# Kernel optimization log

Measured on AMD Instinct MI355X. Metric: run time of the kernel, lower is better.

Reference implementation:

```python
import jax, jax.numpy as jnp
import numpy as np

WINDOW = 8
NUM_HEADS = 12


def setup_inputs() -> dict:
    key = jax.random.key(0)
    k1, k2, k3 = jax.random.split(key, 3)
    B, H, W, C = 32, 64, 64, 384
    x = jax.random.normal(k1, (B, H, W, C), dtype=jnp.float32)
    w_qkv = jax.random.normal(k2, (C, 3 * C), dtype=jnp.float32) * (C ** -0.5)
    w_proj = jax.random.normal(k3, (C, C), dtype=jnp.float32) * (C ** -0.5)
    b_proj = jnp.zeros((C,), dtype=jnp.float32)
    return {"x": x, "w_qkv": w_qkv, "w_proj": w_proj, "b_proj": b_proj}


def window_partition(x, ws):
    B, H, W, C = x.shape
    x = x.reshape(B, H // ws, ws, W // ws, ws, C)
    x = x.transpose(0, 1, 3, 2, 4, 5)  # [B, nH, nW, ws, ws, C]
    return x.reshape(-1, ws * ws, C)


def window_reverse(x, ws, H, W):
    nWin = (H // ws) * (W // ws)
    B = x.shape[0] // nWin
    C = x.shape[2]
    x = x.reshape(B, H // ws, W // ws, ws, ws, C)
    x = x.transpose(0, 1, 3, 2, 4, 5)
    return x.reshape(B, H, W, C)


def reference(x, w_qkv, w_proj, b_proj):
    B, H, W, C = x.shape
    ws = WINDOW
    nh = NUM_HEADS
    hd = C // nh
    scale = hd ** -0.5
    N = ws * ws

    xw = window_partition(x, ws)                      # [nW*B, N, C]
    qkv = xw @ w_qkv                                  # [nW*B, N, 3C]
    qkv = qkv.reshape(-1, N, 3, nh, hd)
    qkv = qkv.transpose(2, 0, 3, 1, 4)                # [3, nW*B, nh, N, hd]
    q, k, v = qkv[0], qkv[1], qkv[2]

    attn = jnp.einsum('whnd,whmd->whnm', q, k) * scale  # [nW*B, nh, N, N]
    attn = jax.nn.softmax(attn, axis=-1)
    out = jnp.einsum('whnm,whmd->whnd', attn, v)         # [nW*B, nh, N, hd]
    out = out.transpose(0, 2, 1, 3).reshape(-1, N, C)    # [nW*B, N, C]
    out = out @ w_proj + b_proj
    return window_reverse(out, ws, H, W)
```

## Files before the change

### kernel.cpp

```cpp
#include <hip/hip_runtime.h>


typedef __attribute__((ext_vector_type(8))) short bf16x8;
typedef __attribute__((ext_vector_type(4))) float f32x4;
typedef __attribute__((ext_vector_type(4))) short short4_t;

__device__ __forceinline__ short f2bf(float f) {
    union { float f; unsigned u; } v; v.f = f;
    unsigned r = v.u + 0x7fffu + ((v.u >> 16) & 1u);
    return (short)(r >> 16);
}

__device__ __forceinline__ unsigned pk2(float a, float b) {
    return ((unsigned)(unsigned short)f2bf(b) << 16) | (unsigned short)f2bf(a);
}

__device__ __forceinline__ f32x4 mfma16(bf16x8 a, bf16x8 b, f32x4 c) {
    return __builtin_amdgcn_mfma_f32_16x16x32_bf16(a, b, c, 0, 0, 0);
}

__device__ __forceinline__ short4_t pack4(f32x4 v) {
    short4_t s;
    s.x = f2bf(v[0]); s.y = f2bf(v[1]); s.z = f2bf(v[2]); s.w = f2bf(v[3]);
    return s;
}

__device__ __forceinline__ void gload_lds16(const void* g, void* l) {
    __builtin_amdgcn_global_load_lds(
        (const __attribute__((address_space(1))) unsigned int*)g,
        (__attribute__((address_space(3))) unsigned int*)l, 16, 0, 0);
}

__global__ void prep_weights(const float* __restrict__ wqkv, const float* __restrict__ wproj,
                             short* __restrict__ wq_sw, short* __restrict__ wp_t) {
    const int QKV_ELEMS = 12 * 96 * 384;
    int i = blockIdx.x * 256 + threadIdx.x;
    if (i < QKV_ELEMS) {
        int h = i / (96 * 384);
        int o = i % (96 * 384);
        int row = o / 384;
        int kb = ((o % 384) * 2) ^ ((row & 7) << 4);
        int k = kb >> 1;
        int col = (row >> 5) * 384 + h * 32 + (row & 31);
        float w = wqkv[k * 1152 + col];
        if (row < 32) w *= 0.17677669529663687f;
        wq_sw[i] = f2bf(w);
    } else if (i < QKV_ELEMS + 384 * 384) {
        int j = i - QKV_ELEMS;
        int n = j / 384, k = j % 384;
        wp_t[j] = f2bf(wproj[k * 384 + n]);
    }
}

__global__ __launch_bounds__(1024, 4)
void qkv_attn(const float* __restrict__ x, const short* __restrict__ wq_sw,
              short* __restrict__ y_sw) {
    __shared__ short Wl[96 * 384];
    __shared__ short k_s[4][64 * 44];
    __shared__ short v_t[4][32 * 76];
    __shared__ short ps[4][64 * 76];

    const int tid   = threadIdx.x;
    const int lane  = tid & 63;
    const int wid   = tid >> 6;
    const int col16 = lane & 15;
    const int kgrp  = lane >> 4;
    const int w     = wid >> 2;
    const int quad  = wid & 3;

    const int win = blockIdx.x * 4 + w;
    const int b = win >> 6, wi = win & 63, whr = wi >> 3, wwc = wi & 7;
    const float* xbase = x + (((b * 64) + whr * 8) * 64 + wwc * 8) * 384;

    for (int i = wid; i < 72; i += 16)
        gload_lds16(wq_sw + i * 512 + lane * 8, &Wl[i * 512]);

    bf16x8 xf[12];
    {
        int t = quad * 16 + col16;
        const float* xr = xbase + ((t >> 3) * 64 + (t & 7)) * 384;
#pragma unroll
        for (int kk = 0; kk < 12; ++kk) {
            const float* p0 = xr + kk * 32 + kgrp * 8;
            float4 a = *reinterpret_cast<const float4*>(p0);
            float4 c = *reinterpret_cast<const float4*>(p0 + 4);
            bf16x8 f;
            f[0] = f2bf(a.x); f[1] = f2bf(a.y); f[2] = f2bf(a.z); f[3] = f2bf(a.w);
            f[4] = f2bf(c.x); f[5] = f2bf(c.y); f[6] = f2bf(c.z); f[7] = f2bf(c.w);
            xf[kk] = f;
        }
    }

    const int g = win * 64 + quad * 16 + col16;
    const int mtile = g >> 7, yrow = g & 127;
    char* ybase = (char*)y_sw + (size_t)mtile * 98304 + (size_t)yrow * 128;

    for (int h = 0; h < 12; ++h) {
        __syncthreads();

        f32x4 acc[6];
#pragma unroll
        for (int i = 0; i < 6; ++i) acc[i] = (f32x4){0.f, 0.f, 0.f, 0.f};
#pragma unroll
        for (int kk = 0; kk < 12; ++kk) {
            const int kbyte = (kk * 32 + kgrp * 8) * 2;
#pragma unroll
            for (int rd = 0; rd < 6; ++rd) {
                const int row = (rd >> 1) * 32 + (rd & 1) * 16 + col16;
                const bf16x8 wf = *reinterpret_cast<const bf16x8*>(
                    (const char*)Wl + row * 768 + (kbyte ^ ((row & 7) << 4)));
                if (rd < 4) acc[rd] = mfma16(wf, xf[kk], acc[rd]);
                else        acc[rd] = mfma16(xf[kk], wf, acc[rd]);
            }
        }
        bf16x8 qa;
        {
            unsigned A0 = pk2(acc[0][0], acc[0][1]);
            unsigned A1 = pk2(acc[0][2], acc[0][3]);
            unsigned B0 = pk2(acc[1][0], acc[1][1]);
            unsigned B1 = pk2(acc[1][2], acc[1][3]);
            int s0 = ((kgrp & 1) * 2) * 16 + col16;
            int a0 = __shfl((int)A0, s0, 64),      a1 = __shfl((int)A1, s0, 64);
            int a2 = __shfl((int)A0, s0 + 16, 64), a3 = __shfl((int)A1, s0 + 16, 64);
            int b0 = __shfl((int)B0, s0, 64),      b1 = __shfl((int)B1, s0, 64);
            int b2 = __shfl((int)B0, s0 + 16, 64), b3 = __shfl((int)B1, s0 + 16, 64);
            union { int i[4]; bf16x8 v; } qu;
            const bool loHalf = (kgrp < 2);
            qu.i[0] = loHalf ? a0 : b0;
            qu.i[1] = loHalf ? a1 : b1;
            qu.i[2] = loHalf ? a2 : b2;
            qu.i[3] = loHalf ? a3 : b3;
            qa = qu.v;
        }
#pragma unroll
        for (int rd = 2; rd < 4; ++rd)
            *reinterpret_cast<short4_t*>(
                &k_s[w][(quad * 16 + col16) * 44 + (rd & 1) * 16 + kgrp * 4]) = pack4(acc[rd]);
#pragma unroll
        for (int d = 0; d < 2; ++d)
            *reinterpret_cast<short4_t*>(
                &v_t[w][(d * 16 + col16) * 76 + quad * 16 + kgrp * 4]) = pack4(acc[4 + d]);

        __syncthreads();

        if (h < 11) {
            const short* src = wq_sw + (h + 1) * (96 * 384);
            for (int i = wid; i < 72; i += 16)
                gload_lds16(src + i * 512 + lane * 8, &Wl[i * 512]);
        }

        f32x4 sc[4];
#pragma unroll
        for (int nt = 0; nt < 4; ++nt) {
            bf16x8 kf = *reinterpret_cast<const bf16x8*>(
                &k_s[w][(nt * 16 + col16) * 44 + kgrp * 8]);
            f32x4 z = (f32x4){0.f, 0.f, 0.f, 0.f};
            sc[nt] = mfma16(qa, kf, z);
        }
        float mx[4], sm[4];
#pragma unroll
        for (int r = 0; r < 4; ++r)
            mx[r] = fmaxf(fmaxf(sc[0][r], sc[1][r]), fmaxf(sc[2][r], sc[3][r]));
#pragma unroll
        for (int d = 1; d < 16; d <<= 1)
#pragma unroll
            for (int r = 0; r < 4; ++r) mx[r] = fmaxf(mx[r], __shfl_xor(mx[r], d, 16));
#pragma unroll
        for (int r = 0; r < 4; ++r) {
            sm[r] = 0.f;
#pragma unroll
            for (int nt = 0; nt < 4; ++nt) {
                sc[nt][r] = __expf(sc[nt][r] - mx[r]); sm[r] += sc[nt][r];
            }
        }
#pragma unroll
        for (int d = 1; d < 16; d <<= 1)
#pragma unroll
            for (int r = 0; r < 4; ++r) sm[r] += __shfl_xor(sm[r], d, 16);
#pragma unroll
        for (int r = 0; r < 4; ++r) {
            float inv = 1.0f / sm[r];
            int prow = quad * 16 + kgrp * 4 + r;
#pragma unroll
            for (int nt = 0; nt < 4; ++nt)
                ps[w][prow * 76 + nt * 16 + col16] = f2bf(sc[nt][r] * inv);
        }
        f32x4 o2[2];
        o2[0] = (f32x4){0.f, 0.f, 0.f, 0.f};
        o2[1] = (f32x4){0.f, 0.f, 0.f, 0.f};
#pragma unroll
        for (int kt = 0; kt < 2; ++kt) {
            bf16x8 pb = *reinterpret_cast<const bf16x8*>(
                &ps[w][(quad * 16 + col16) * 76 + kt * 32 + kgrp * 8]);
#pragma unroll
            for (int d = 0; d < 2; ++d) {
                bf16x8 va = *reinterpret_cast<const bf16x8*>(
                    &v_t[w][(d * 16 + col16) * 76 + kt * 32 + kgrp * 8]);
                o2[d] = mfma16(va, pb, o2[d]);
            }
        }
#pragma unroll
        for (int d = 0; d < 2; ++d) {
            int c0 = h * 32 + d * 16 + kgrp * 4;
            int kchunk = c0 >> 6;
            int koff = (2 * (c0 & 63)) ^ ((yrow & 7) << 4);
            *reinterpret_cast<short4_t*>(ybase + kchunk * 16384 + koff) = pack4(o2[d]);
        }
    }
}

__global__ __launch_bounds__(256)
void proj_gemm(const short* __restrict__ y_sw, const short* __restrict__ wp_t,
               const float* __restrict__ b_proj, float* __restrict__ out) {
    __shared__ short At[2][128 * 64];

    const int tid = threadIdx.x, lane = tid & 63, wv = tid >> 6;
    const int col16 = lane & 15, kgrp = lane >> 4;
    const int wm = wv >> 1, wn = wv & 1;
    const int mtile = blockIdx.x;
    const int nblk  = blockIdx.y;

    const short* asrc = y_sw + (size_t)mtile * 6 * 128 * 64;

    for (int i = wv; i < 16; i += 4)
        gload_lds16(asrc + i * 512 + lane * 8, &At[0][i * 512]);

    const short* bptr[4];
#pragma unroll
    for (int nt = 0; nt < 4; ++nt)
        bptr[nt] = wp_t + (size_t)(nblk * 128 + wn * 64 + nt * 16 + col16) * 384;

    f32x4 acc[4][4];
#pragma unroll
    for (int i = 0; i < 4; ++i)
#pragma unroll
        for (int j = 0; j < 4; ++j) acc[i][j] = (f32x4){0.f, 0.f, 0.f, 0.f};

    int cur = 0;
    for (int ks = 0; ks < 6; ++ks) {
        __syncthreads();
        if (ks < 5) {
            const short* src = asrc + (ks + 1) * (128 * 64);
            for (int i = wv; i < 16; i += 4)
                gload_lds16(src + i * 512 + lane * 8, &At[cur ^ 1][i * 512]);
        }
#pragma unroll
        for (int kk = 0; kk < 2; ++kk) {
            const int kbyte = kk * 64 + kgrp * 16;
            bf16x8 af[4];
#pragma unroll
            for (int mt = 0; mt < 4; ++mt) {
                const int r = wm * 64 + mt * 16 + col16;
                af[mt] = *reinterpret_cast<const bf16x8*>(
                    (const char*)At[cur] + r * 128 + (kbyte ^ ((r & 7) << 4)));
            }
#pragma unroll
            for (int nt = 0; nt < 4; ++nt) {
                bf16x8 bf = *reinterpret_cast<const bf16x8*>(bptr[nt] + ks * 64 + kk * 32 + kgrp * 8);
#pragma unroll
                for (int mt = 0; mt < 4; ++mt)
                    acc[mt][nt] = mfma16(af[mt], bf, acc[mt][nt]);
            }
        }
        cur ^= 1;
    }

#pragma unroll
    for (int nt = 0; nt < 4; ++nt) {
        int c = nblk * 128 + wn * 64 + nt * 16 + col16;
        float bias = b_proj[c];
#pragma unroll
        for (int mt = 0; mt < 4; ++mt) {
#pragma unroll
            for (int r = 0; r < 4; ++r) {
                int gg = mtile * 128 + wm * 64 + mt * 16 + kgrp * 4 + r;
                int win = gg >> 6, t = gg & 63;
                int b = win >> 6, whr = (win >> 3) & 7, wwc = win & 7;
                int orow = (b * 64 + whr * 8 + (t >> 3)) * 64 + wwc * 8 + (t & 7);
                out[(size_t)orow * 384 + c] = acc[mt][nt][r] + bias;
            }
        }
    }
}

__global__ __launch_bounds__(512, 2)
void win_attn_fused(const float* __restrict__ x, const short* __restrict__ wq_sw,
                    const short* __restrict__ wp_t, const float* __restrict__ b_proj,
                    float* __restrict__ out) {
    __shared__ short Wl[96 * 384];
    __shared__ short q_s[2][64 * 40];
    __shared__ short k_s[2][64 * 40];
    __shared__ short v_t[2][32 * 72];
    __shared__ short ps[2][64 * 72];

    const int tid   = threadIdx.x;
    const int lane  = tid & 63;
    const int wv    = tid >> 6;
    const int col16 = lane & 15;
    const int kgrp  = lane >> 4;
    const int wwin  = wv >> 2;
    const int q4    = wv & 3;
    const int wm    = q4 >> 1, wn = q4 & 1;

    const int win = blockIdx.x * 2 + wwin;
    const int b = win >> 6, wi = win & 63, whr = wi >> 3, wwc = wi & 7;
    const float* xbase = x + (((b * 64) + whr * 8) * 64 + wwc * 8) * 384;

    for (int i = 0; i < 9; ++i) {
        int chunk = wv * 9 + i;
        gload_lds16(wq_sw + chunk * 512 + lane * 8, &Wl[chunk * 512]);
    }
    bf16x8 xf[12];
    {
        int t = q4 * 16 + col16;
        const float* xr = xbase + ((t >> 3) * 64 + (t & 7)) * 384;
#pragma unroll
        for (int kk = 0; kk < 12; ++kk) {
            const float* p0 = xr + kk * 32 + kgrp * 8;
            float4 a = *reinterpret_cast<const float4*>(p0);
            float4 c = *reinterpret_cast<const float4*>(p0 + 4);
            bf16x8 f;
            f[0] = f2bf(a.x); f[1] = f2bf(a.y); f[2] = f2bf(a.z); f[3] = f2bf(a.w);
            f[4] = f2bf(c.x); f[5] = f2bf(c.y); f[6] = f2bf(c.z); f[7] = f2bf(c.w);
            xf[kk] = f;
        }
    }
    f32x4 pacc[2][12];
#pragma unroll
    for (int i = 0; i < 2; ++i)
#pragma unroll
        for (int j = 0; j < 12; ++j) pacc[i][j] = (f32x4){0.f, 0.f, 0.f, 0.f};

    for (int h = 0; h < 12; ++h) {
        __syncthreads();
        f32x4 acc[6];
#pragma unroll
        for (int i = 0; i < 6; ++i) acc[i] = (f32x4){0.f, 0.f, 0.f, 0.f};
#pragma unroll
        for (int kk = 0; kk < 12; ++kk) {
            const int kbyte = (kk * 32 + kgrp * 8) * 2;
#pragma unroll
            for (int rd = 0; rd < 6; ++rd) {
                const int row = (rd >> 1) * 32 + (rd & 1) * 16 + col16;
                const bf16x8 wf = *reinterpret_cast<const bf16x8*>(
                    (const char*)Wl + row * 768 + (kbyte ^ ((row & 7) << 4)));
                if (rd < 4) acc[rd] = mfma16(wf, xf[kk], acc[rd]);
                else        acc[rd] = mfma16(xf[kk], wf, acc[rd]);
            }
        }
#pragma unroll
        for (int rd = 0; rd < 4; ++rd) {
            short* dst = (rd < 2) ? q_s[wwin] : k_s[wwin];
            *reinterpret_cast<short4_t*>(
                &dst[(q4 * 16 + col16) * 40 + (rd & 1) * 16 + kgrp * 4]) = pack4(acc[rd]);
        }
#pragma unroll
        for (int d = 0; d < 2; ++d)
            *reinterpret_cast<short4_t*>(
                &v_t[wwin][(d * 16 + col16) * 72 + q4 * 16 + kgrp * 4]) = pack4(acc[4 + d]);

        __syncthreads();
        if (h < 11) {
            const short* src = wq_sw + (h + 1) * (96 * 384);
            for (int i = 0; i < 9; ++i) {
                int chunk = wv * 9 + i;
                gload_lds16(src + chunk * 512 + lane * 8, &Wl[chunk * 512]);
            }
        }
        bf16x8 qa = *reinterpret_cast<const bf16x8*>(
            &q_s[wwin][(q4 * 16 + col16) * 40 + kgrp * 8]);
        f32x4 sc[4];
#pragma unroll
        for (int nt = 0; nt < 4; ++nt) {
            bf16x8 kf = *reinterpret_cast<const bf16x8*>(
                &k_s[wwin][(nt * 16 + col16) * 40 + kgrp * 8]);
            f32x4 z = (f32x4){0.f, 0.f, 0.f, 0.f};
            sc[nt] = mfma16(qa, kf, z);
        }
        float mx[4], sm[4], p[4][4];
#pragma unroll
        for (int r = 0; r < 4; ++r)
            mx[r] = fmaxf(fmaxf(sc[0][r], sc[1][r]), fmaxf(sc[2][r], sc[3][r]));
#pragma unroll
        for (int d = 1; d < 16; d <<= 1)
#pragma unroll
            for (int r = 0; r < 4; ++r) mx[r] = fmaxf(mx[r], __shfl_xor(mx[r], d, 16));
#pragma unroll
        for (int r = 0; r < 4; ++r) {
            sm[r] = 0.f;
#pragma unroll
            for (int nt = 0; nt < 4; ++nt) { p[nt][r] = __expf(sc[nt][r] - mx[r]); sm[r] += p[nt][r]; }
        }
#pragma unroll
        for (int d = 1; d < 16; d <<= 1)
#pragma unroll
            for (int r = 0; r < 4; ++r) sm[r] += __shfl_xor(sm[r], d, 16);
#pragma unroll
        for (int r = 0; r < 4; ++r) {
            float inv = 1.0f / sm[r];
            int prow = q4 * 16 + kgrp * 4 + r;
#pragma unroll
            for (int nt = 0; nt < 4; ++nt)
                ps[wwin][prow * 72 + nt * 16 + col16] = f2bf(p[nt][r] * inv);
        }
        f32x4 o2[2];
        o2[0] = (f32x4){0.f, 0.f, 0.f, 0.f};
        o2[1] = (f32x4){0.f, 0.f, 0.f, 0.f};
#pragma unroll
        for (int kt = 0; kt < 2; ++kt) {
            bf16x8 pb = *reinterpret_cast<const bf16x8*>(
                &ps[wwin][(q4 * 16 + col16) * 72 + kt * 32 + kgrp * 8]);
#pragma unroll
            for (int d = 0; d < 2; ++d) {
                bf16x8 va = *reinterpret_cast<const bf16x8*>(
                    &v_t[wwin][(d * 16 + col16) * 72 + kt * 32 + kgrp * 8]);
                o2[d] = mfma16(va, pb, o2[d]);
            }
        }
#pragma unroll
        for (int d = 0; d < 2; ++d)
            *reinterpret_cast<short4_t*>(
                &ps[wwin][(q4 * 16 + col16) * 72 + d * 16 + kgrp * 4]) = pack4(o2[d]);
        __syncthreads();
#pragma unroll
        for (int mt = 0; mt < 2; ++mt) {
            bf16x8 ya = *reinterpret_cast<const bf16x8*>(
                &ps[wwin][(wm * 32 + mt * 16 + col16) * 72 + kgrp * 8]);
#pragma unroll
            for (int nt = 0; nt < 12; ++nt) {
                bf16x8 wb = *reinterpret_cast<const bf16x8*>(
                    &wp_t[(wn * 192 + nt * 16 + col16) * 384 + h * 32 + kgrp * 8]);
                pacc[mt][nt] = mfma16(ya, wb, pacc[mt][nt]);
            }
        }
    }
#pragma unroll
    for (int nt = 0; nt < 12; ++nt) {
        int c = wn * 192 + nt * 16 + col16;
        float bias = b_proj[c];
#pragma unroll
        for (int mt = 0; mt < 2; ++mt) {
#pragma unroll
            for (int r = 0; r < 4; ++r) {
                int token = wm * 32 + mt * 16 + kgrp * 4 + r;
                int hh = whr * 8 + (token >> 3);
                int ww2 = wwc * 8 + (token & 7);
                out[(((b * 64) + hh) * 64 + ww2) * 384 + c] = pacc[mt][nt][r] + bias;
            }
        }
    }
}

extern "C" void kernel_launch(void* const* d_in, const int* in_sizes, int n_in,
                              void* d_out, int out_size, void* d_ws, size_t ws_size,
                              hipStream_t stream) {
    const float* x     = (const float*)d_in[0];
    const float* wqkv  = (const float*)d_in[1];
    const float* wproj = (const float*)d_in[2];
    const float* bproj = (const float*)d_in[3];

    short* wq_sw = (short*)d_ws;
    short* wp_t  = wq_sw + 12 * 96 * 384;
    short* y_sw  = wp_t + 384 * 384;
    const size_t need = (size_t)(12 * 96 * 384 + 384 * 384) * 2 + (size_t)1024 * 6 * 128 * 128;

    prep_weights<<<2304, 256, 0, stream>>>(wqkv, wproj, wq_sw, wp_t);
    if (ws_size >= need) {
        qkv_attn<<<512, 1024, 0, stream>>>(x, wq_sw, y_sw);
        proj_gemm<<<dim3(1024, 3), 256, 0, stream>>>(y_sw, wp_t, bproj, (float*)d_out);
    } else {
        win_attn_fused<<<1024, 512, 0, stream>>>(x, wq_sw, wp_t, bproj, (float*)d_out);
    }
}
```

Baseline: 391.2 us.

## Halve qkv_attn block to two windows and split per-head weight staging

After: 379.8 us. 2.9% less time.

```diff
diff --git a/kernel.cpp b/kernel.cpp
--- a/kernel.cpp
+++ b/kernel.cpp
@@ -29,6 +29,11 @@
     __builtin_amdgcn_global_load_lds(
         (const __attribute__((address_space(1))) unsigned int*)g,
         (__attribute__((address_space(3))) unsigned int*)l, 16, 0, 0);
+}
+
+__device__ __forceinline__ void drain_vmem() {
+    asm volatile("s_waitcnt vmcnt(0)" ::: "memory");
+    __builtin_amdgcn_sched_barrier(0);
 }
 
 __global__ void prep_weights(const float* __restrict__ wqkv, const float* __restrict__ wproj,
@@ -52,13 +57,13 @@
     }
 }
 
-__global__ __launch_bounds__(1024, 4)
+__global__ __launch_bounds__(512, 4)
 void qkv_attn(const float* __restrict__ x, const short* __restrict__ wq_sw,
               short* __restrict__ y_sw) {
-    __shared__ short Wl[96 * 384];
-    __shared__ short k_s[4][64 * 44];
-    __shared__ short v_t[4][32 * 76];
-    __shared__ short ps[4][64 * 76];
+    __shared__ short Wl[48 * 384];
+    __shared__ short k_s[2][64 * 40];
+    __shared__ short v_t[2][32 * 72];
+    __shared__ short ps[2][64 * 72];
 
     const int tid   = threadIdx.x;
     const int lane  = tid & 63;
@@ -68,11 +73,11 @@
     const int w     = wid >> 2;
     const int quad  = wid & 3;
 
-    const int win = blockIdx.x * 4 + w;
+    const int win = blockIdx.x * 2 + w;
     const int b = win >> 6, wi = win & 63, whr = wi >> 3, wwc = wi & 7;
     const float* xbase = x + (((b * 64) + whr * 8) * 64 + wwc * 8) * 384;
 
-    for (int i = wid; i < 72; i += 16)
+    for (int i = wid; i < 36; i += 8)
         gload_lds16(wq_sw + i * 512 + lane * 8, &Wl[i * 512]);
 
     bf16x8 xf[12];
@@ -96,29 +101,41 @@
     char* ybase = (char*)y_sw + (size_t)mtile * 98304 + (size_t)yrow * 128;
 
     for (int h = 0; h < 12; ++h) {
-        __syncthreads();
-
-        f32x4 acc[6];
-#pragma unroll
-        for (int i = 0; i < 6; ++i) acc[i] = (f32x4){0.f, 0.f, 0.f, 0.f};
+        drain_vmem();
+        __syncthreads();
+
+        f32x4 aQ0 = (f32x4){0.f, 0.f, 0.f, 0.f};
+        f32x4 aQ1 = (f32x4){0.f, 0.f, 0.f, 0.f};
+        f32x4 aK0 = (f32x4){0.f, 0.f, 0.f, 0.f};
 #pragma unroll
         for (int kk = 0; kk < 12; ++kk) {
             const int kbyte = (kk * 32 + kgrp * 8) * 2;
-#pragma unroll
-            for (int rd = 0; rd < 6; ++rd) {
-                const int row = (rd >> 1) * 32 + (rd & 1) * 16 + col16;
-                const bf16x8 wf = *reinterpret_cast<const bf16x8*>(
-                    (const char*)Wl + row * 768 + (kbyte ^ ((row & 7) << 4)));
-                if (rd < 4) acc[rd] = mfma16(wf, xf[kk], acc[rd]);
-                else        acc[rd] = mfma16(xf[kk], wf, acc[rd]);
-            }
-        }
+            const int r0 = col16, r1 = 16 + col16, r2 = 32 + col16;
+            bf16x8 wf0 = *reinterpret_cast<const bf16x8*>(
+                (const char*)Wl + r0 * 768 + (kbyte ^ ((r0 & 7) << 4)));
+            bf16x8 wf1 = *reinterpret_cast<const bf16x8*>(
+                (const char*)Wl + r1 * 768 + (kbyte ^ ((r1 & 7) << 4)));
+            bf16x8 wf2 = *reinterpret_cast<const bf16x8*>(
+                (const char*)Wl + r2 * 768 + (kbyte ^ ((r2 & 7) << 4)));
+            aQ0 = mfma16(wf0, xf[kk], aQ0);
+            aQ1 = mfma16(wf1, xf[kk], aQ1);
+            aK0 = mfma16(wf2, xf[kk], aK0);
+        }
+
+        __syncthreads();
+
+        {
+            const short* src = wq_sw + h * (96 * 384) + 48 * 384;
+            for (int i = wid; i < 36; i += 8)
+                gload_lds16(src + i * 512 + lane * 8, &Wl[i * 512]);
+        }
+
         bf16x8 qa;
         {
-            unsigned A0 = pk2(acc[0][0], acc[0][1]);
-            unsigned A1 = pk2(acc[0][2], acc[0][3]);
-            unsigned B0 = pk2(acc[1][0], acc[1][1]);
-            unsigned B1 = pk2(acc[1][2], acc[1][3]);
+            unsigned A0 = pk2(aQ0[0], aQ0[1]);
+            unsigned A1 = pk2(aQ0[2], aQ0[3]);
+            unsigned B0 = pk2(aQ1[0], aQ1[1]);
+            unsigned B1 = pk2(aQ1[2], aQ1[3]);
             int s0 = ((kgrp & 1) * 2) * 16 + col16;
             int a0 = __shfl((int)A0, s0, 64),      a1 = __shfl((int)A1, s0, 64);
             int a2 = __shfl((int)A0, s0 + 16, 64), a3 = __shfl((int)A1, s0 + 16, 64);
@@ -132,20 +149,41 @@
             qu.i[3] = loHalf ? a3 : b3;
             qa = qu.v;
         }
-#pragma unroll
-        for (int rd = 2; rd < 4; ++rd)
-            *reinterpret_cast<short4_t*>(
-                &k_s[w][(quad * 16 + col16) * 44 + (rd & 1) * 16 + kgrp * 4]) = pack4(acc[rd]);
-#pragma unroll
-        for (int d = 0; d < 2; ++d)
-            *reinterpret_cast<short4_t*>(
-                &v_t[w][(d * 16 + col16) * 76 + quad * 16 + kgrp * 4]) = pack4(acc[4 + d]);
+        *reinterpret_cast<short4_t*>(
+            &k_s[w][(quad * 16 + col16) * 40 + kgrp * 4]) = pack4(aK0);
+
+        drain_vmem();
+        __syncthreads();
+
+        f32x4 aK1 = (f32x4){0.f, 0.f, 0.f, 0.f};
+        f32x4 aV0 = (f32x4){0.f, 0.f, 0.f, 0.f};
+        f32x4 aV1 = (f32x4){0.f, 0.f, 0.f, 0.f};
+#pragma unroll
+        for (int kk = 0; kk < 12; ++kk) {
+            const int kbyte = (kk * 32 + kgrp * 8) * 2;
+            const int r0 = col16, r1 = 16 + col16, r2 = 32 + col16;
+            bf16x8 wfK = *reinterpret_cast<const bf16x8*>(
+                (const char*)Wl + r0 * 768 + (kbyte ^ ((r0 & 7) << 4)));
+            bf16x8 wfV0 = *reinterpret_cast<const bf16x8*>(
+                (const char*)Wl + r1 * 768 + (kbyte ^ ((r1 & 7) << 4)));
+            bf16x8 wfV1 = *reinterpret_cast<const bf16x8*>(
+                (const char*)Wl + r2 * 768 + (kbyte ^ ((r2 & 7) << 4)));
+            aK1 = mfma16(wfK, xf[kk], aK1);
+            aV0 = mfma16(xf[kk], wfV0, aV0);
+            aV1 = mfma16(xf[kk], wfV1, aV1);
+        }
+        *reinterpret_cast<short4_t*>(
+            &k_s[w][(quad * 16 + col16) * 40 + 16 + kgrp * 4]) = pack4(aK1);
+        *reinterpret_cast<short4_t*>(
+            &v_t[w][(col16) * 72 + quad * 16 + kgrp * 4]) = pack4(aV0);
+        *reinterpret_cast<short4_t*>(
+            &v_t[w][(16 + col16) * 72 + quad * 16 + kgrp * 4]) = pack4(aV1);
 
         __syncthreads();
 
         if (h < 11) {
             const short* src = wq_sw + (h + 1) * (96 * 384);
-            for (int i = wid; i < 72; i += 16)
+            for (int i = wid; i < 36; i += 8)
                 gload_lds16(src + i * 512 + lane * 8, &Wl[i * 512]);
         }
 
@@ -153,7 +191,7 @@
 #pragma unroll
         for (int nt = 0; nt < 4; ++nt) {
             bf16x8 kf = *reinterpret_cast<const bf16x8*>(
-                &k_s[w][(nt * 16 + col16) * 44 + kgrp * 8]);
+                &k_s[w][(nt * 16 + col16) * 40 + kgrp * 8]);
             f32x4 z = (f32x4){0.f, 0.f, 0.f, 0.f};
             sc[nt] = mfma16(qa, kf, z);
         }
@@ -183,7 +221,7 @@
             int prow = quad * 16 + kgrp * 4 + r;
 #pragma unroll
             for (int nt = 0; nt < 4; ++nt)
-                ps[w][prow * 76 + nt * 16 + col16] = f2bf(sc[nt][r] * inv);
+                ps[w][prow * 72 + nt * 16 + col16] = f2bf(sc[nt][r] * inv);
         }
         f32x4 o2[2];
         o2[0] = (f32x4){0.f, 0.f, 0.f, 0.f};
@@ -191,11 +229,11 @@
 #pragma unroll
         for (int kt = 0; kt < 2; ++kt) {
             bf16x8 pb = *reinterpret_cast<const bf16x8*>(
-                &ps[w][(quad * 16 + col16) * 76 + kt * 32 + kgrp * 8]);
+                &ps[w][(quad * 16 + col16) * 72 + kt * 32 + kgrp * 8]);
 #pragma unroll
             for (int d = 0; d < 2; ++d) {
                 bf16x8 va = *reinterpret_cast<const bf16x8*>(
-                    &v_t[w][(d * 16 + col16) * 76 + kt * 32 + kgrp * 8]);
+                    &v_t[w][(d * 16 + col16) * 72 + kt * 32 + kgrp * 8]);
                 o2[d] = mfma16(va, pb, o2[d]);
             }
         }
@@ -238,6 +276,7 @@
 
     int cur = 0;
     for (int ks = 0; ks < 6; ++ks) {
+        drain_vmem();
         __syncthreads();
         if (ks < 5) {
             const short* src = asrc + (ks + 1) * (128 * 64);
@@ -332,6 +371,7 @@
         for (int j = 0; j < 12; ++j) pacc[i][j] = (f32x4){0.f, 0.f, 0.f, 0.f};
 
     for (int h = 0; h < 12; ++h) {
+        drain_vmem();
         __syncthreads();
         f32x4 acc[6];
 #pragma unroll
@@ -466,7 +506,7 @@
 
     prep_weights<<<2304, 256, 0, stream>>>(wqkv, wproj, wq_sw, wp_t);
     if (ws_size >= need) {
-        qkv_attn<<<512, 1024, 0, stream>>>(x, wq_sw, y_sw);
+        qkv_attn<<<1024, 512, 0, stream>>>(x, wq_sw, y_sw);
         proj_gemm<<<dim3(1024, 3), 256, 0, stream>>>(y_sw, wp_t, bproj, (float*)d_out);
     } else {
         win_attn_fused<<<1024, 512, 0, stream>>>(x, wq_sw, wp_t, bproj, (float*)d_out);
```
